# Kernel tuning notes

Measured on AMD Instinct MI355X. Metric: run time of the kernel, lower is better.

## Reference

```python
import jax, jax.numpy as jnp
import numpy as np
import math

ITER = 5
ALPHA = 2.0
C = 128
B, H, W = 64, 40, 96


def _conv(x, w, pad_h, pad_w):
    # x: [B,C,H,W], w: [O,I,kh,kw]
    return jax.lax.conv_general_dilated(
        x, w, window_strides=(1, 1),
        padding=[(pad_h, pad_h), (pad_w, pad_w)],
        dimension_numbers=("NCHW", "OIHW", "NCHW"))


def setup_inputs() -> dict:
    key = jax.random.key(0)
    k = jax.random.split(key, 5)
    bound = math.sqrt(2.0 / (C * 9 * 5))
    x = jax.random.normal(k[0], (B, C, H, W), dtype=jnp.float32)
    wd = jax.random.uniform(k[1], (ITER, C, C, 1, 9), jnp.float32, -bound, bound)
    wu = jax.random.uniform(k[2], (ITER, C, C, 1, 9), jnp.float32, -bound, bound)
    wr = jax.random.uniform(k[3], (ITER, C, C, 9, 1), jnp.float32, -bound, bound)
    wl = jax.random.uniform(k[4], (ITER, C, C, 9, 1), jnp.float32, -bound, bound)
    return {"x": x, "wd": wd, "wu": wu, "wr": wr, "wl": wl}


def reference(x, wd, wu, wr, wl):
    h, w = x.shape[-2], x.shape[-1]
    y = x
    # downward: circular shift of rows by +offset == roll(-offset) along H
    for i in range(ITER):
        off = h // 2 ** (ITER - i)
        y = y + ALPHA * jax.nn.relu(_conv(jnp.roll(y, -off, axis=2), wd[i], 0, 4))
    # upward: rows shifted by -offset == roll(+offset)
    for i in range(ITER):
        off = h // 2 ** (ITER - i)
        y = y + ALPHA * jax.nn.relu(_conv(jnp.roll(y, off, axis=2), wu[i], 0, 4))
    # rightward: cols shifted by +offset == roll(-offset) along W
    for i in range(ITER):
        off = w // 2 ** (ITER - i)
        y = y + ALPHA * jax.nn.relu(_conv(jnp.roll(y, -off, axis=3), wr[i], 4, 0))
    # leftward: cols shifted by -offset == roll(+offset)
    for i in range(ITER):
        off = w // 2 ** (ITER - i)
        y = y + ALPHA * jax.nn.relu(_conv(jnp.roll(y, off, axis=3), wl[i], 4, 0))
    return y
```

## Files before the change

### kernel.cpp

```cpp
#include <hip/hip_runtime.h>
#include <cstdint>
#include <cstddef>

#define CH 128
#define HH 40
#define WW 96
#define BB 64
#define HW (HH*WW)
#define CHW ((size_t)CH*HW)

typedef _Float16 half8  __attribute__((ext_vector_type(8)));
typedef _Float16 half4v __attribute__((ext_vector_type(4)));
typedef float    float4v __attribute__((ext_vector_type(4)));

#define MFMA16(a,b,c) __builtin_amdgcn_mfma_f32_16x16x32_f16((a),(b),(c),0,0,0)

#define SPLIT_SCALE 2048.0f
#define INV_SPLIT   (1.0f/2048.0f)

#define NHWC_HALVES (BB*HH*WW*CH)
#define WSTEP_F     (CH*CH*9)
#define WFRAG_HALVES (20*9*4*8*64*8)


__global__ __launch_bounds__(256) void prep_weights(
    const float* __restrict__ wd, const float* __restrict__ wu,
    const float* __restrict__ wr, const float* __restrict__ wl,
    _Float16* __restrict__ WH, _Float16* __restrict__ WM)
{
    const int bx = blockIdx.x;
    const int s = bx / 9, t = bx % 9;
    const float* src;
    if (s < 5)       src = wd + (size_t)s*WSTEP_F;
    else if (s < 10) src = wu + (size_t)(s-5)*WSTEP_F;
    else if (s < 15) src = wr + (size_t)(s-10)*WSTEP_F;
    else             src = wl + (size_t)(s-15)*WSTEP_F;

    for (int idx = threadIdx.x; idx < 2048; idx += 256) {
        const int lane = idx & 63;
        const int mt   = (idx >> 6) & 7;
        const int kq   = idx >> 9;
        const int co   = mt*16 + (lane & 15);
        const int cib  = kq*32 + (lane >> 4)*8;
        const int F    = ((((s*9 + t)*4 + kq)*8 + mt)*64 + lane)*8;
        #pragma unroll
        for (int j = 0; j < 8; ++j) {
            const float w = src[(size_t)(co*CH + (cib + j))*9 + t];
            const _Float16 h = (_Float16)w;
            WH[F + j] = h;
            WM[F + j] = (_Float16)((w - (float)h) * SPLIT_SCALE);
        }
    }
}

__global__ __launch_bounds__(256) void prep_acts(
    const float* __restrict__ x, _Float16* __restrict__ H, _Float16* __restrict__ M)
{
    __shared__ float tile[CH][33];
    const int wt = blockIdx.x, h = blockIdx.y, b = blockIdx.z;
    const int tid = threadIdx.x;
    {
        const int wl = tid & 31, c0 = tid >> 5;
        for (int it = 0; it < 16; ++it) {
            const int ci = it*8 + c0;
            tile[ci][wl] = x[((size_t)(b*CH + ci)*HH + h)*WW + wt*32 + wl];
        }
    }
    __syncthreads();
    {
        const int ci = tid & 127, w0 = tid >> 7;
        for (int it = 0; it < 16; ++it) {
            const int wl = it*2 + w0;
            const float v = tile[ci][wl];
            const _Float16 hh = (_Float16)v;
            const int o = ((b*HH + h)*WW + wt*32 + wl)*CH + ci;
            H[o] = hh;
            M[o] = (_Float16)((v - (float)hh) * SPLIT_SCALE);
        }
    }
}

__global__ __launch_bounds__(256, 2) void hconv_mfma(
    const _Float16* __restrict__ srcH, const _Float16* __restrict__ srcM,
    _Float16* __restrict__ dstH, _Float16* __restrict__ dstM,
    const _Float16* __restrict__ WH, const _Float16* __restrict__ WM,
    int s, int hoff)
{
    __shared__ _Float16 sB[2][104*136];
    const int h = blockIdx.x, b = blockIdx.y;
    const int tid = threadIdx.x;
    const int hp = (h + hoff) % HH;

    {
        const int l = tid & 15, r0 = tid >> 4;
        for (int it = 0; it < 7; ++it) {
            const int r = it*16 + r0;
            if (r < 104) {
                half8 vh = {}, vm = {};
                if (r >= 4 && r < 100) {
                    const int off = ((b*HH + hp)*WW + (r-4))*CH + l*8;
                    vh = *(const half8*)(srcH + off);
                    vm = *(const half8*)(srcM + off);
                }
                *(half8*)&sB[0][r*136 + l*8] = vh;
                *(half8*)&sB[1][r*136 + l*8] = vm;
            }
        }
    }
    __syncthreads();

    const int lane = tid & 63, wave = tid >> 6;
    const int n = lane & 15, quad = lane >> 4;
    const int mgrp = wave & 1, ngrp = wave >> 1;

    float4v acc0[4][3], acc1[4][3];
    #pragma unroll
    for (int i = 0; i < 4; ++i)
        #pragma unroll
        for (int j = 0; j < 3; ++j) {
            acc0[i][j] = (float4v){0.f,0.f,0.f,0.f};
            acc1[i][j] = (float4v){0.f,0.f,0.f,0.f};
        }

    int rowb[3];
    #pragma unroll
    for (int j = 0; j < 3; ++j) rowb[j] = (ngrp*3 + j)*16 + n;

    for (int t = 0; t < 9; ++t) {
        for (int kq = 0; kq < 4; ++kq) {
            const int F = ((((s*9 + t)*4 + kq)*8 + mgrp*4)*64 + lane)*8;
            half8 AH[4], AM[4];
            #pragma unroll
            for (int i = 0; i < 4; ++i) {
                AH[i] = *(const half8*)(WH + F + i*512);
                AM[i] = *(const half8*)(WM + F + i*512);
            }
            #pragma unroll
            for (int j = 0; j < 3; ++j) {
                const int ro = (rowb[j] + t)*136 + kq*32 + quad*8;
                const half8 bh = *(const half8*)&sB[0][ro];
                const half8 bm = *(const half8*)&sB[1][ro];
                #pragma unroll
                for (int i = 0; i < 4; ++i) {
                    acc0[i][j] = MFMA16(AH[i], bh, acc0[i][j]);
                    acc1[i][j] = MFMA16(AH[i], bm, acc1[i][j]);
                    acc1[i][j] = MFMA16(AM[i], bh, acc1[i][j]);
                }
            }
        }
    }

    const int spbase = (b*HH + h)*WW;
    #pragma unroll
    for (int i = 0; i < 4; ++i) {
        const int co = (mgrp*4 + i)*16 + quad*4;
        #pragma unroll
        for (int j = 0; j < 3; ++j) {
            const int w  = (ngrp*3 + j)*16 + n;
            const int sp = (spbase + w)*CH + co;
            const half4v oh = *(const half4v*)(srcH + sp);
            const half4v om = *(const half4v*)(srcM + sp);
            half4v zh, zm;
            #pragma unroll
            for (int r = 0; r < 4; ++r) {
                const float v = acc0[i][j][r] + acc1[i][j][r]*INV_SPLIT;
                const float y = (float)oh[r] + (float)om[r]*INV_SPLIT;
                const float z = y + 2.0f*fmaxf(v, 0.0f);
                const _Float16 a = (_Float16)z;
                zh[r] = a;
                zm[r] = (_Float16)((z - (float)a)*SPLIT_SCALE);
            }
            *(half4v*)(dstH + sp) = zh;
            *(half4v*)(dstM + sp) = zm;
        }
    }
}

__global__ __launch_bounds__(256, 2) void vconv_mfma(
    const _Float16* __restrict__ srcH, const _Float16* __restrict__ srcM,
    _Float16* __restrict__ dstH, _Float16* __restrict__ dstM,
    const _Float16* __restrict__ WH, const _Float16* __restrict__ WM,
    int s, int woff, int final, float* __restrict__ f32out)
{
    __shared__ _Float16 sB[2][2*56*136];
    const int wp = blockIdx.x, b = blockIdx.y;
    const int tid = threadIdx.x;

    {
        const int l = tid & 15, r0 = tid >> 4;
        for (int it = 0; it < 7; ++it) {
            const int r = it*16 + r0;
            const int col = r / 56, p = r % 56;
            half8 vh = {}, vm = {};
            if (p >= 4 && p < 44) {
                const int wsrc = (wp*2 + col + woff) % WW;
                const int off = ((b*HH + (p-4))*WW + wsrc)*CH + l*8;
                vh = *(const half8*)(srcH + off);
                vm = *(const half8*)(srcM + off);
            }
            *(half8*)&sB[0][(col*56 + p)*136 + l*8] = vh;
            *(half8*)&sB[1][(col*56 + p)*136 + l*8] = vm;
        }
    }
    __syncthreads();

    const int lane = tid & 63, wave = tid >> 6;
    const int n = lane & 15, quad = lane >> 4;
    const int mgrp = wave & 1, col = wave >> 1;

    float4v acc0[4][3], acc1[4][3];
    #pragma unroll
    for (int i = 0; i < 4; ++i)
        #pragma unroll
        for (int j = 0; j < 3; ++j) {
            acc0[i][j] = (float4v){0.f,0.f,0.f,0.f};
            acc1[i][j] = (float4v){0.f,0.f,0.f,0.f};
        }

    int rowb[3];
    #pragma unroll
    for (int j = 0; j < 3; ++j) rowb[j] = col*56 + j*16 + n;

    for (int t = 0; t < 9; ++t) {
        for (int kq = 0; kq < 4; ++kq) {
            const int F = ((((s*9 + t)*4 + kq)*8 + mgrp*4)*64 + lane)*8;
            half8 AH[4], AM[4];
            #pragma unroll
            for (int i = 0; i < 4; ++i) {
                AH[i] = *(const half8*)(WH + F + i*512);
                AM[i] = *(const half8*)(WM + F + i*512);
            }
            #pragma unroll
            for (int j = 0; j < 3; ++j) {
                const int ro = (rowb[j] + t)*136 + kq*32 + quad*8;
                const half8 bh = *(const half8*)&sB[0][ro];
                const half8 bm = *(const half8*)&sB[1][ro];
                #pragma unroll
                for (int i = 0; i < 4; ++i) {
                    acc0[i][j] = MFMA16(AH[i], bh, acc0[i][j]);
                    acc1[i][j] = MFMA16(AH[i], bm, acc1[i][j]);
                    acc1[i][j] = MFMA16(AM[i], bh, acc1[i][j]);
                }
            }
        }
    }

    const int w_out = wp*2 + col;
    #pragma unroll
    for (int i = 0; i < 4; ++i) {
        const int co = (mgrp*4 + i)*16 + quad*4;
        #pragma unroll
        for (int j = 0; j < 3; ++j) {
            const int h_out = j*16 + n;
            if (h_out < HH) {
                const int sp = ((b*HH + h_out)*WW + w_out)*CH + co;
                const half4v oh = *(const half4v*)(srcH + sp);
                const half4v om = *(const half4v*)(srcM + sp);
                if (final) {
                    float4v z4;
                    #pragma unroll
                    for (int r = 0; r < 4; ++r) {
                        const float v = acc0[i][j][r] + acc1[i][j][r]*INV_SPLIT;
                        const float y = (float)oh[r] + (float)om[r]*INV_SPLIT;
                        z4[r] = y + 2.0f*fmaxf(v, 0.0f);
                    }
                    *(float4v*)(f32out + sp) = z4;
                } else {
                    half4v zh, zm;
                    #pragma unroll
                    for (int r = 0; r < 4; ++r) {
                        const float v = acc0[i][j][r] + acc1[i][j][r]*INV_SPLIT;
                        const float y = (float)oh[r] + (float)om[r]*INV_SPLIT;
                        const float z = y + 2.0f*fmaxf(v, 0.0f);
                        const _Float16 a = (_Float16)z;
                        zh[r] = a;
                        zm[r] = (_Float16)((z - (float)a)*SPLIT_SCALE);
                    }
                    *(half4v*)(dstH + sp) = zh;
                    *(half4v*)(dstM + sp) = zm;
                }
            }
        }
    }
}

__global__ __launch_bounds__(256) void nhwc_to_nchw(
    const float* __restrict__ src, float* __restrict__ dst)
{
    __shared__ float tile[32][133];
    const int wt = blockIdx.x, h = blockIdx.y, b = blockIdx.z;
    const int tid = threadIdx.x;
    {
        const int ci = tid & 127, w0 = tid >> 7;
        for (int it = 0; it < 16; ++it) {
            const int wl = it*2 + w0;
            tile[wl][ci] = src[((size_t)(b*HH + h)*WW + wt*32 + wl)*CH + ci];
        }
    }
    __syncthreads();
    {
        const int wl = tid & 31, c0 = tid >> 5;
        for (int it = 0; it < 16; ++it) {
            const int ci = it*8 + c0;
            dst[((size_t)(b*CH + ci)*HH + h)*WW + wt*32 + wl] = tile[wl][ci];
        }
    }
}

__global__ __launch_bounds__(256) void hconv_step(
    const float* __restrict__ src, const float* __restrict__ wgt,
    float* __restrict__ dst, int hoff)
{
    __shared__ float ld[CH][104];
    const int h = blockIdx.x, b = blockIdx.y, tid = threadIdx.x;
    const int hp = (h + hoff) % HH;
    const float* srow = src + (size_t)b*CHW + (size_t)hp*WW;
    for (int idx = tid; idx < CH*24; idx += 256) {
        int ci = idx / 24, j = idx % 24;
        float4 v = *reinterpret_cast<const float4*>(srow + (size_t)ci*HW + j*4);
        *reinterpret_cast<float4*>(&ld[ci][4 + 4*j]) = v;
    }
    if (tid < CH) {
        *reinterpret_cast<float4*>(&ld[tid][0])   = make_float4(0.f,0.f,0.f,0.f);
        *reinterpret_cast<float4*>(&ld[tid][100]) = make_float4(0.f,0.f,0.f,0.f);
    }
    __syncthreads();
    const int tx = tid & 7, ty = tid >> 3;
    const int w0 = tx*12, co0 = ty*4;
    float acc[4][12];
    #pragma unroll
    for (int c = 0; c < 4; ++c)
        #pragma unroll
        for (int k = 0; k < 12; ++k) acc[c][k] = 0.f;
    const float* wb = wgt + (size_t)co0*(CH*9);
    for (int ci = 0; ci < CH; ++ci) {
        float xr[20];
        #pragma unroll
        for (int j = 0; j < 5; ++j) {
            float4 v = *reinterpret_cast<const float4*>(&ld[ci][w0 + 4*j]);
            xr[4*j+0]=v.x; xr[4*j+1]=v.y; xr[4*j+2]=v.z; xr[4*j+3]=v.w;
        }
        #pragma unroll
        for (int c = 0; c < 4; ++c) {
            const float* wp = wb + (size_t)c*(CH*9) + ci*9;
            #pragma unroll
            for (int t = 0; t < 9; ++t) {
                const float wv = wp[t];
                #pragma unroll
                for (int k = 0; k < 12; ++k) acc[c][k] = fmaf(wv, xr[k+t], acc[c][k]);
            }
        }
    }
    const size_t obase = (size_t)b*CHW + (size_t)h*WW + w0;
    #pragma unroll
    for (int c = 0; c < 4; ++c) {
        const size_t o = obase + (size_t)(co0 + c)*HW;
        #pragma unroll
        for (int j = 0; j < 3; ++j) {
            float4 s = *reinterpret_cast<const float4*>(src + o + 4*j);
            float4 r;
            r.x = s.x + 2.f*fmaxf(acc[c][4*j+0], 0.f);
            r.y = s.y + 2.f*fmaxf(acc[c][4*j+1], 0.f);
            r.z = s.z + 2.f*fmaxf(acc[c][4*j+2], 0.f);
            r.w = s.w + 2.f*fmaxf(acc[c][4*j+3], 0.f);
            *reinterpret_cast<float4*>(dst + o + 4*j) = r;
        }
    }
}

__global__ __launch_bounds__(256) void vconv_step(
    const float* __restrict__ src, const float* __restrict__ wgt,
    float* __restrict__ dst, int woff)
{
    __shared__ float ld[CH][2][48];
    const int w0 = blockIdx.x*2, b = blockIdx.y, tid = threadIdx.x;
    const int w1 = (w0 + woff) % WW, w2 = (w0 + 1 + woff) % WW;
    const float* sb = src + (size_t)b*CHW;
    for (int idx = tid; idx < CH*HH; idx += 256) {
        int ci = idx / HH, hh = idx % HH;
        const float* p = sb + (size_t)ci*HW + (size_t)hh*WW;
        ld[ci][0][4 + hh] = p[w1];
        ld[ci][1][4 + hh] = p[w2];
    }
    if (tid < CH) {
        #pragma unroll
        for (int j = 0; j < 4; ++j) {
            ld[tid][0][j]=0.f; ld[tid][0][44+j]=0.f;
            ld[tid][1][j]=0.f; ld[tid][1][44+j]=0.f;
        }
    }
    __syncthreads();
    const int tx = tid & 7, ty = tid >> 3;
    const int wi = tx >> 2, h0 = (tx & 3)*10, co0 = ty*4;
    float acc[4][10];
    #pragma unroll
    for (int c = 0; c < 4; ++c)
        #pragma unroll
        for (int k = 0; k < 10; ++k) acc[c][k] = 0.f;
    const float* wb = wgt + (size_t)co0*(CH*9);
    for (int ci = 0; ci < CH; ++ci) {
        float xr[18];
        #pragma unroll
        for (int j = 0; j < 18; ++j) xr[j] = ld[ci][wi][h0 + j];
        #pragma unroll
        for (int c = 0; c < 4; ++c) {
            const float* wp = wb + (size_t)c*(CH*9) + ci*9;
            #pragma unroll
            for (int t = 0; t < 9; ++t) {
                const float wv = wp[t];
                #pragma unroll
                for (int k = 0; k < 10; ++k) acc[c][k] = fmaf(wv, xr[k+t], acc[c][k]);
            }
        }
    }
    #pragma unroll
    for (int c = 0; c < 4; ++c) {
        const size_t o = (size_t)b*CHW + (size_t)(co0 + c)*HW + (size_t)h0*WW + (w0 + wi);
        #pragma unroll
        for (int k = 0; k < 10; ++k) {
            const float s = src[o + (size_t)k*WW];
            dst[o + (size_t)k*WW] = s + 2.f*fmaxf(acc[c][k], 0.f);
        }
    }
}

extern "C" void kernel_launch(void* const* d_in, const int* in_sizes, int n_in,
                              void* d_out, int out_size, void* d_ws, size_t ws_size,
                              hipStream_t stream)
{
    const float* x  = (const float*)d_in[0];
    const float* wd = (const float*)d_in[1];
    const float* wu = (const float*)d_in[2];
    const float* wr = (const float*)d_in[3];
    const float* wl = (const float*)d_in[4];

    const size_t NEED = 125829120ULL + 2ULL*WFRAG_HALVES*2ULL;

    if (ws_size >= NEED) {
        _Float16* HA  = (_Float16*)d_ws;
        _Float16* MA  = HA + NHWC_HALVES;
        _Float16* WHp = (_Float16*)((char*)d_ws + 125829120ULL);
        _Float16* WMp = WHp + WFRAG_HALVES;
        _Float16* HB  = (_Float16*)d_out;
        _Float16* MB  = HB + NHWC_HALVES;
        float* f32tmp = (float*)d_ws;

        prep_weights<<<dim3(180), 256, 0, stream>>>(wd, wu, wr, wl, WHp, WMp);
        prep_acts<<<dim3(3, HH, BB), 256, 0, stream>>>(x, HA, MA);

        const int hoffs[10] = {1,2,5,10,20, 39,38,35,30,20};
        for (int s = 0; s < 10; ++s) {
            const _Float16* sH = (s & 1) ? HB : HA;
            const _Float16* sM = (s & 1) ? MB : MA;
            _Float16* dH = (s & 1) ? HA : HB;
            _Float16* dM = (s & 1) ? MA : MB;
            hconv_mfma<<<dim3(HH, BB), 256, 0, stream>>>(sH, sM, dH, dM,
                                                         WHp, WMp, s, hoffs[s]);
        }
        const int woffs[10] = {3,6,12,24,48, 93,90,84,72,48};
        for (int k = 0; k < 10; ++k) {
            const int s = 10 + k;
            const _Float16* sH = (s & 1) ? HB : HA;
            const _Float16* sM = (s & 1) ? MB : MA;
            _Float16* dH = (s & 1) ? HA : HB;
            _Float16* dM = (s & 1) ? MA : MB;
            const int fin = (s == 19);
            vconv_mfma<<<dim3(WW/2, BB), 256, 0, stream>>>(sH, sM, dH, dM,
                                                           WHp, WMp, s, woffs[k],
                                                           fin, f32tmp);
        }
        nhwc_to_nchw<<<dim3(3, HH, BB), 256, 0, stream>>>(f32tmp, (float*)d_out);
    } else {
        float* out = (float*)d_out;
        float* ws  = (float*)d_ws;
        const size_t WSTEP = (size_t)WSTEP_F;
        const int hoffs[5] = {1, 2, 5, 10, 20};
        const int woffs[5] = {3, 6, 12, 24, 48};
        dim3 hgrid(HH, BB), vgrid(WW/2, BB);
        const float* src = x;
        int step = 0;
        for (int i = 0; i < 5; ++i) {
            float* dst = (step & 1) ? out : ws;
            hconv_step<<<hgrid, 256, 0, stream>>>(src, wd + i*WSTEP, dst, hoffs[i]);
            src = dst; ++step;
        }
        for (int i = 0; i < 5; ++i) {
            float* dst = (step & 1) ? out : ws;
            hconv_step<<<hgrid, 256, 0, stream>>>(src, wu + i*WSTEP, dst, (HH - hoffs[i]) % HH);
            src = dst; ++step;
        }
        for (int i = 0; i < 5; ++i) {
            float* dst = (step & 1) ? out : ws;
            vconv_step<<<vgrid, 256, 0, stream>>>(src, wr + i*WSTEP, dst, woffs[i]);
            src = dst; ++step;
        }
        for (int i = 0; i < 5; ++i) {
            float* dst = (step & 1) ? out : ws;
            vconv_step<<<vgrid, 256, 0, stream>>>(src, wl + i*WSTEP, dst, (WW - woffs[i]) % WW);
            src = dst; ++step;
        }
    }
}
```

Baseline: 4.995 ms.

## Switch conv kernels to 32x32x16 MFMA with swizzled LDS and tighter padding

Replaces the 16x16x32 MFMA tiling with 32x32x16 MFMA, so each wave owns 32 output channels across three 32-wide N tiles. Weight fragments are re-laid out to match, and LDS uses an XOR swizzle in place of row padding. The vertical kernel packs two columns' 40 rows into three 32-row tiles, which cuts wasted padded rows. Occupancy hint rises to 3 blocks per CU. The aim is fewer MFMA issues and register-held A fragments, fewer LDS bank conflicts, and less wasted compute, at the cost of more complex index mapping.

```diff
diff --git a/kernel.cpp b/kernel.cpp
--- a/kernel.cpp
+++ b/kernel.cpp
@@ -9,18 +9,19 @@
 #define HW (HH*WW)
 #define CHW ((size_t)CH*HW)
 
-typedef _Float16 half8  __attribute__((ext_vector_type(8)));
-typedef _Float16 half4v __attribute__((ext_vector_type(4)));
+typedef _Float16 half8   __attribute__((ext_vector_type(8)));
+typedef _Float16 half4v  __attribute__((ext_vector_type(4)));
 typedef float    float4v __attribute__((ext_vector_type(4)));
-
-#define MFMA16(a,b,c) __builtin_amdgcn_mfma_f32_16x16x32_f16((a),(b),(c),0,0,0)
+typedef float    float16v __attribute__((ext_vector_type(16)));
+
+#define MFMA32(a,b,c) __builtin_amdgcn_mfma_f32_32x32x16_f16((a),(b),(c),0,0,0)
 
 #define SPLIT_SCALE 2048.0f
 #define INV_SPLIT   (1.0f/2048.0f)
 
 #define NHWC_HALVES (BB*HH*WW*CH)
 #define WSTEP_F     (CH*CH*9)
-#define WFRAG_HALVES (20*9*4*8*64*8)
+#define WFRAG_HALVES (20*9*8*4*64*8)
 
 
 __global__ __launch_bounds__(256) void prep_weights(
@@ -38,11 +39,11 @@
 
     for (int idx = threadIdx.x; idx < 2048; idx += 256) {
         const int lane = idx & 63;
-        const int mt   = (idx >> 6) & 7;
-        const int kq   = idx >> 9;
-        const int co   = mt*16 + (lane & 15);
-        const int cib  = kq*32 + (lane >> 4)*8;
-        const int F    = ((((s*9 + t)*4 + kq)*8 + mt)*64 + lane)*8;
+        const int mt   = (idx >> 6) & 3;
+        const int kq   = idx >> 8;
+        const int co   = mt*32 + (lane & 31);
+        const int cib  = kq*16 + (lane >> 5)*8;
+        const int F    = ((((s*9 + t)*8 + kq)*4 + mt)*64 + lane)*8;
         #pragma unroll
         for (int j = 0; j < 8; ++j) {
             const float w = src[(size_t)(co*CH + (cib + j))*9 + t];
@@ -80,90 +81,78 @@
     }
 }
 
-__global__ __launch_bounds__(256, 2) void hconv_mfma(
+__global__ __launch_bounds__(256, 3) void hconv_mfma(
     const _Float16* __restrict__ srcH, const _Float16* __restrict__ srcM,
     _Float16* __restrict__ dstH, _Float16* __restrict__ dstM,
     const _Float16* __restrict__ WH, const _Float16* __restrict__ WM,
     int s, int hoff)
 {
-    __shared__ _Float16 sB[2][104*136];
+    __shared__ _Float16 sB[2][104*128];
     const int h = blockIdx.x, b = blockIdx.y;
     const int tid = threadIdx.x;
     const int hp = (h + hoff) % HH;
 
     {
-        const int l = tid & 15, r0 = tid >> 4;
-        for (int it = 0; it < 7; ++it) {
-            const int r = it*16 + r0;
-            if (r < 104) {
-                half8 vh = {}, vm = {};
-                if (r >= 4 && r < 100) {
-                    const int off = ((b*HH + hp)*WW + (r-4))*CH + l*8;
-                    vh = *(const half8*)(srcH + off);
-                    vm = *(const half8*)(srcM + off);
-                }
-                *(half8*)&sB[0][r*136 + l*8] = vh;
-                *(half8*)&sB[1][r*136 + l*8] = vm;
-            }
+        const int l = tid & 15, rr = tid >> 4;
+        #pragma unroll
+        for (int it = 0; it < 13; ++it) {
+            const int slot = it*16 + rr;
+            const int part = slot >= 104;
+            const int r    = slot - part*104;
+            half8 v = {};
+            if (r >= 4 && r < 100) {
+                const _Float16* sp = part ? srcM : srcH;
+                v = *(const half8*)(sp + ((b*HH + hp)*WW + (r-4))*CH + l*8);
+            }
+            *(half8*)&sB[part][r*128 + ((l ^ (r & 15))*8)] = v;
         }
     }
     __syncthreads();
 
     const int lane = tid & 63, wave = tid >> 6;
-    const int n = lane & 15, quad = lane >> 4;
-    const int mgrp = wave & 1, ngrp = wave >> 1;
-
-    float4v acc0[4][3], acc1[4][3];
-    #pragma unroll
-    for (int i = 0; i < 4; ++i)
-        #pragma unroll
-        for (int j = 0; j < 3; ++j) {
-            acc0[i][j] = (float4v){0.f,0.f,0.f,0.f};
-            acc1[i][j] = (float4v){0.f,0.f,0.f,0.f};
-        }
-
-    int rowb[3];
-    #pragma unroll
-    for (int j = 0; j < 3; ++j) rowb[j] = (ngrp*3 + j)*16 + n;
+    const int n  = lane & 31;
+    const int q2 = lane >> 5;
+
+    float16v acc0[3], acc1[3];
+    #pragma unroll
+    for (int j = 0; j < 3; ++j) {
+        acc0[j] = (float16v)(0.0f);
+        acc1[j] = (float16v)(0.0f);
+    }
 
     for (int t = 0; t < 9; ++t) {
-        for (int kq = 0; kq < 4; ++kq) {
-            const int F = ((((s*9 + t)*4 + kq)*8 + mgrp*4)*64 + lane)*8;
-            half8 AH[4], AM[4];
-            #pragma unroll
-            for (int i = 0; i < 4; ++i) {
-                AH[i] = *(const half8*)(WH + F + i*512);
-                AM[i] = *(const half8*)(WM + F + i*512);
-            }
+        #pragma unroll 2
+        for (int kq = 0; kq < 8; ++kq) {
+            const int F = ((((s*9 + t)*8 + kq)*4 + wave)*64 + lane)*8;
+            const half8 AH = *(const half8*)(WH + F);
+            const half8 AM = *(const half8*)(WM + F);
             #pragma unroll
             for (int j = 0; j < 3; ++j) {
-                const int ro = (rowb[j] + t)*136 + kq*32 + quad*8;
-                const half8 bh = *(const half8*)&sB[0][ro];
-                const half8 bm = *(const half8*)&sB[1][ro];
-                #pragma unroll
-                for (int i = 0; i < 4; ++i) {
-                    acc0[i][j] = MFMA16(AH[i], bh, acc0[i][j]);
-                    acc1[i][j] = MFMA16(AH[i], bm, acc1[i][j]);
-                    acc1[i][j] = MFMA16(AM[i], bh, acc1[i][j]);
-                }
+                const int row = j*32 + n + t;
+                const int off = row*128 + (((kq*2 + q2) ^ (row & 15))*8);
+                const half8 bh = *(const half8*)&sB[0][off];
+                const half8 bm = *(const half8*)&sB[1][off];
+                acc0[j] = MFMA32(AH, bh, acc0[j]);
+                acc1[j] = MFMA32(AH, bm, acc1[j]);
+                acc1[j] = MFMA32(AM, bh, acc1[j]);
             }
         }
     }
 
     const int spbase = (b*HH + h)*WW;
     #pragma unroll
-    for (int i = 0; i < 4; ++i) {
-        const int co = (mgrp*4 + i)*16 + quad*4;
-        #pragma unroll
-        for (int j = 0; j < 3; ++j) {
-            const int w  = (ngrp*3 + j)*16 + n;
+    for (int j = 0; j < 3; ++j) {
+        const int w = j*32 + n;
+        #pragma unroll
+        for (int g = 0; g < 4; ++g) {
+            const int co = wave*32 + g*8 + q2*4;
             const int sp = (spbase + w)*CH + co;
             const half4v oh = *(const half4v*)(srcH + sp);
             const half4v om = *(const half4v*)(srcM + sp);
             half4v zh, zm;
             #pragma unroll
             for (int r = 0; r < 4; ++r) {
-                const float v = acc0[i][j][r] + acc1[i][j][r]*INV_SPLIT;
+                const float v = acc0[j][g*4+r] + acc1[j][g*4+r]*INV_SPLIT;
                 const float y = (float)oh[r] + (float)om[r]*INV_SPLIT;
                 const float z = y + 2.0f*fmaxf(v, 0.0f);
                 const _Float16 a = (_Float16)z;
@@ -176,83 +165,80 @@
     }
 }
 
-__global__ __launch_bounds__(256, 2) void vconv_mfma(
+__global__ __launch_bounds__(256, 3) void vconv_mfma(
     const _Float16* __restrict__ srcH, const _Float16* __restrict__ srcM,
     _Float16* __restrict__ dstH, _Float16* __restrict__ dstM,
     const _Float16* __restrict__ WH, const _Float16* __restrict__ WM,
     int s, int woff, int final, float* __restrict__ f32out)
 {
-    __shared__ _Float16 sB[2][2*56*136];
+    __shared__ _Float16 sB[2][96*128];
     const int wp = blockIdx.x, b = blockIdx.y;
     const int tid = threadIdx.x;
 
     {
-        const int l = tid & 15, r0 = tid >> 4;
-        for (int it = 0; it < 7; ++it) {
-            const int r = it*16 + r0;
-            const int col = r / 56, p = r % 56;
-            half8 vh = {}, vm = {};
+        const int l = tid & 15, rr = tid >> 4;
+        #pragma unroll
+        for (int it = 0; it < 12; ++it) {
+            const int slot = it*16 + rr;
+            const int part = slot >= 96;
+            const int r    = slot - part*96;
+            const int col  = r / 48, p = r % 48;
+            half8 v = {};
             if (p >= 4 && p < 44) {
                 const int wsrc = (wp*2 + col + woff) % WW;
-                const int off = ((b*HH + (p-4))*WW + wsrc)*CH + l*8;
-                vh = *(const half8*)(srcH + off);
-                vm = *(const half8*)(srcM + off);
-            }
-            *(half8*)&sB[0][(col*56 + p)*136 + l*8] = vh;
-            *(half8*)&sB[1][(col*56 + p)*136 + l*8] = vm;
+                const _Float16* spr = part ? srcM : srcH;
+                v = *(const half8*)(spr + ((b*HH + (p-4))*WW + wsrc)*CH + l*8);
+            }
+            *(half8*)&sB[part][r*128 + ((l ^ (r & 15))*8)] = v;
         }
     }
     __syncthreads();
 
     const int lane = tid & 63, wave = tid >> 6;
-    const int n = lane & 15, quad = lane >> 4;
-    const int mgrp = wave & 1, col = wave >> 1;
-
-    float4v acc0[4][3], acc1[4][3];
-    #pragma unroll
-    for (int i = 0; i < 4; ++i)
-        #pragma unroll
-        for (int j = 0; j < 3; ++j) {
-            acc0[i][j] = (float4v){0.f,0.f,0.f,0.f};
-            acc1[i][j] = (float4v){0.f,0.f,0.f,0.f};
-        }
+    const int n  = lane & 31;
+    const int q2 = lane >> 5;
 
     int rowb[3];
-    #pragma unroll
-    for (int j = 0; j < 3; ++j) rowb[j] = col*56 + j*16 + n;
+    rowb[0] = n;
+    rowb[1] = 48 + n;
+    rowb[2] = (n < 8) ? (32 + n) : (n < 16 ? (72 + n) : 0);
+
+    float16v acc0[3], acc1[3];
+    #pragma unroll
+    for (int j = 0; j < 3; ++j) {
+        acc0[j] = (float16v)(0.0f);
+        acc1[j] = (float16v)(0.0f);
+    }
 
     for (int t = 0; t < 9; ++t) {
-        for (int kq = 0; kq < 4; ++kq) {
-            const int F = ((((s*9 + t)*4 + kq)*8 + mgrp*4)*64 + lane)*8;
-            half8 AH[4], AM[4];
-            #pragma unroll
-            for (int i = 0; i < 4; ++i) {
-                AH[i] = *(const half8*)(WH + F + i*512);
-                AM[i] = *(const half8*)(WM + F + i*512);
-            }
+        #pragma unroll 2
+        for (int kq = 0; kq < 8; ++kq) {
+            const int F = ((((s*9 + t)*8 + kq)*4 + wave)*64 + lane)*8;
+            const half8 AH = *(const half8*)(WH + F);
+            const half8 AM = *(const half8*)(WM + F);
             #pragma unroll
             for (int j = 0; j < 3; ++j) {
-                const int ro = (rowb[j] + t)*136 + kq*32 + quad*8;
-                const half8 bh = *(const half8*)&sB[0][ro];
-                const half8 bm = *(const half8*)&sB[1][ro];
-                #pragma unroll
-                for (int i = 0; i < 4; ++i) {
-                    acc0[i][j] = MFMA16(AH[i], bh, acc0[i][j]);
-                    acc1[i][j] = MFMA16(AH[i], bm, acc1[i][j]);
-                    acc1[i][j] = MFMA16(AM[i], bh, acc1[i][j]);
-                }
-            }
-        }
-    }
-
-    const int w_out = wp*2 + col;
-    #pragma unroll
-    for (int i = 0; i < 4; ++i) {
-        const int co = (mgrp*4 + i)*16 + quad*4;
-        #pragma unroll
-        for (int j = 0; j < 3; ++j) {
-            const int h_out = j*16 + n;
-            if (h_out < HH) {
+                const int row = rowb[j] + t;
+                const int off = row*128 + (((kq*2 + q2) ^ (row & 15))*8);
+                const half8 bh = *(const half8*)&sB[0][off];
+                const half8 bm = *(const half8*)&sB[1][off];
+                acc0[j] = MFMA32(AH, bh, acc0[j]);
+                acc1[j] = MFMA32(AH, bm, acc1[j]);
+                acc1[j] = MFMA32(AM, bh, acc1[j]);
+            }
+        }
+    }
+
+    #pragma unroll
+    for (int j = 0; j < 3; ++j) {
+        int h_out, w_out, valid = 1;
+        if (j < 2)      { h_out = n;            w_out = wp*2 + j; }
+        else if (n < 16){ h_out = 32 + (n & 7); w_out = wp*2 + (n >> 3); }
+        else            { valid = 0; h_out = 0; w_out = 0; }
+        if (valid) {
+            #pragma unroll
+            for (int g = 0; g < 4; ++g) {
+                const int co = wave*32 + g*8 + q2*4;
                 const int sp = ((b*HH + h_out)*WW + w_out)*CH + co;
                 const half4v oh = *(const half4v*)(srcH + sp);
                 const half4v om = *(const half4v*)(srcM + sp);
@@ -260,7 +246,7 @@
                     float4v z4;
                     #pragma unroll
                     for (int r = 0; r < 4; ++r) {
-                        const float v = acc0[i][j][r] + acc1[i][j][r]*INV_SPLIT;
+                        const float v = acc0[j][g*4+r] + acc1[j][g*4+r]*INV_SPLIT;
                         const float y = (float)oh[r] + (float)om[r]*INV_SPLIT;
                         z4[r] = y + 2.0f*fmaxf(v, 0.0f);
                     }
@@ -269,7 +255,7 @@
                     half4v zh, zm;
                     #pragma unroll
                     for (int r = 0; r < 4; ++r) {
-                        const float v = acc0[i][j][r] + acc1[i][j][r]*INV_SPLIT;
+                        const float v = acc0[j][g*4+r] + acc1[j][g*4+r]*INV_SPLIT;
                         const float y = (float)oh[r] + (float)om[r]*INV_SPLIT;
                         const float z = y + 2.0f*fmaxf(v, 0.0f);
                         const _Float16 a = (_Float16)z;
```

Result: slower. 5.802 ms (+16.1%).
